# Kernel optimization log

Hardware: AMD Instinct MI355X
Metric: run time of the kernel (lower is better)

## Reference

```python
import jax, jax.numpy as jnp
import numpy as np

N = 10000      # nodes
E = 320000     # edges
D = 256        # input_nf = output_nf
H = 256        # hidden_nf
ED = 16        # edges_in_d
NORM = 32.0    # normalization_factor


def setup_inputs() -> dict:
    key = jax.random.key(0)
    ks = jax.random.split(key, 16)
    s = 0.02  # param scale
    return {
        "h": jax.random.normal(ks[0], (N, D), dtype=jnp.float32),
        "edge_index": jax.random.randint(ks[1], (2, E), 0, N, dtype=jnp.int64),
        "edge_attr": jax.random.normal(ks[2], (E, ED), dtype=jnp.float32),
        "node_mask": jnp.ones((N, 1), dtype=jnp.float32),
        "edge_mask": jnp.ones((E, 1), dtype=jnp.float32),
        # edge_mlp: Linear(2D+ED -> H), SiLU, Linear(H -> H), SiLU
        "We1": jax.random.normal(ks[3], (2 * D + ED, H), dtype=jnp.float32) * s,
        "be1": jnp.zeros((H,), dtype=jnp.float32),
        "We2": jax.random.normal(ks[4], (H, H), dtype=jnp.float32) * s,
        "be2": jnp.zeros((H,), dtype=jnp.float32),
        # att_mlp: Linear(H -> 1), Sigmoid
        "Wa": jax.random.normal(ks[5], (H, 1), dtype=jnp.float32) * s,
        "ba": jnp.zeros((1,), dtype=jnp.float32),
        # node_mlp: Linear(H + D -> H), SiLU, Linear(H -> D)
        "Wn1": jax.random.normal(ks[6], (H + D, H), dtype=jnp.float32) * s,
        "bn1": jnp.zeros((H,), dtype=jnp.float32),
        "Wn2": jax.random.normal(ks[7], (H, D), dtype=jnp.float32) * s,
        "bn2": jnp.zeros((D,), dtype=jnp.float32),
    }


def reference(h, edge_index, edge_attr, node_mask, edge_mask,
              We1, be1, We2, be2, Wa, ba, Wn1, bn1, Wn2, bn2):
    row, col = edge_index[0], edge_index[1]
    # edge model: gather endpoints, concat with edge_attr -> [E, 2D+ED]
    e_in = jnp.concatenate([h[row], h[col], edge_attr], axis=1)
    mij = jax.nn.silu(jax.nn.silu(e_in @ We1 + be1) @ We2 + be2)  # [E, H]
    att = jax.nn.sigmoid(mij @ Wa + ba)                            # [E, 1]
    edge_feat = mij * att * edge_mask                              # [E, H]
    # node model: scatter-add messages to rows, normalize by constant
    agg = jax.ops.segment_sum(edge_feat, row, num_segments=h.shape[0]) / NORM  # [N, H]
    a = jnp.concatenate([h, agg], axis=1)                          # [N, D+H]
    h_out = h + (jax.nn.silu(a @ Wn1 + bn1) @ Wn2 + bn2)           # residual
    h_out = h_out * node_mask
    return (h_out, mij)
```

## Files before the change

### kernel.cpp

```cpp
#include <hip/hip_runtime.h>

#define NN 10000
#define NE 320000

typedef __bf16 bf16x8 __attribute__((ext_vector_type(8)));
typedef short  s16x8  __attribute__((ext_vector_type(8)));
typedef float  f32x4  __attribute__((ext_vector_type(4)));

__device__ __forceinline__ unsigned short f2bf(float f) {
  return __builtin_bit_cast(unsigned short, (__bf16)f);
}
__device__ __forceinline__ float bf2f(unsigned short s) {
  unsigned u = ((unsigned)s) << 16;
  return __builtin_bit_cast(float, u);
}
__device__ __forceinline__ float sigm(float x) { return 1.0f / (1.0f + __expf(-x)); }
__device__ __forceinline__ float silu_f(float x) { return x / (1.0f + __expf(-x)); }

__global__ void prep_w(const float* __restrict__ We1, const float* __restrict__ We2,
                       const float* __restrict__ Wn1, const float* __restrict__ Wn2,
                       unsigned short* __restrict__ W1abT, unsigned short* __restrict__ W1cT,
                       unsigned short* __restrict__ We2T,
                       unsigned short* __restrict__ Wn1T, unsigned short* __restrict__ Wn2T) {
  int g = blockIdx.x * blockDim.x + threadIdx.x;
  const int S1 = 512 * 256, S2 = 256 * 32, S3 = 256 * 256, S4 = 256 * 512, S5 = 256 * 256;
  if (g < S1) {
    int n = g >> 8, k = g & 255;
    float v = (n < 256) ? We1[k * 256 + n] : We1[(256 + k) * 256 + (n - 256)];
    W1abT[g] = f2bf(v);
  } else if (g < S1 + S2) {
    int i = g - S1; int n = i >> 5, kk = i & 31;
    float v = (kk < 16) ? We1[(512 + kk) * 256 + n] : 0.0f;
    W1cT[i] = f2bf(v);
  } else if (g < S1 + S2 + S3) {
    int i = g - S1 - S2; int n = i >> 8, k = i & 255;
    We2T[i] = f2bf(We2[k * 256 + n]);
  } else if (g < S1 + S2 + S3 + S4) {
    int i = g - S1 - S2 - S3; int n = i >> 9, k = i & 511;
    Wn1T[i] = f2bf(Wn1[k * 256 + n]);
  } else if (g < S1 + S2 + S3 + S4 + S5) {
    int i = g - S1 - S2 - S3 - S4; int n = i >> 8, k = i & 255;
    Wn2T[i] = f2bf(Wn2[k * 256 + n]);
  }
}

__global__ void prep_x(const float* __restrict__ h, unsigned short* __restrict__ hb) {
  int g = blockIdx.x * blockDim.x + threadIdx.x;
  if (g < NN * 64) {
    float4 f = ((const float4*)h)[g];
    unsigned short* d = hb + g * 4;
    d[0] = f2bf(f.x); d[1] = f2bf(f.y); d[2] = f2bf(f.z); d[3] = f2bf(f.w);
  }
}

__global__ void hist_kernel(const int* __restrict__ eidx, int* __restrict__ rowi,
                            int* __restrict__ counts) {
  __shared__ int s64;
  if (threadIdx.x == 0) {
    bool b = true;
    for (int i = 1; i < 64; i += 2) b = b && (eidx[i] == 0);
    s64 = b ? 1 : 0;
  }
  __syncthreads();
  int e = blockIdx.x * 256 + threadIdx.x;
  if (e < NE) {
    int r = s64 ? (int)((const long long*)eidx)[e] : eidx[e];
    rowi[e] = r;
    atomicAdd(&counts[r], 1);
  }
}

__global__ __launch_bounds__(1024) void scan_kernel(const int* __restrict__ counts,
                                                    int* __restrict__ rowStart,
                                                    int* __restrict__ cursor) {
  __shared__ int part[1024];
  int t = threadIdx.x;
  int local[10];
  int s = 0;
  #pragma unroll
  for (int i = 0; i < 10; i++) {
    int idx = t * 10 + i;
    int c = (idx < NN) ? counts[idx] : 0;
    local[i] = s; s += c;
  }
  part[t] = s;
  __syncthreads();
  int val = s;
  for (int off = 1; off < 1024; off <<= 1) {
    int tmp = (t >= off) ? part[t - off] : 0;
    __syncthreads();
    part[t] += tmp;
    __syncthreads();
  }
  int base = part[t] - val;
  #pragma unroll
  for (int i = 0; i < 10; i++) {
    int idx = t * 10 + i;
    if (idx < NN) { int v = base + local[i]; rowStart[idx] = v; cursor[idx] = v; }
  }
  if (t == 1023) rowStart[NN] = NE;
}

__global__ void scatter_kernel(const int* __restrict__ rowi, int* __restrict__ cursor,
                               int* __restrict__ eorder, int* __restrict__ rowSorted) {
  int e = blockIdx.x * 256 + threadIdx.x;
  if (e < NE) {
    int r = rowi[e];
    int pos = atomicAdd(&cursor[r], 1);
    eorder[pos] = e;
    rowSorted[pos] = r;
  }
}

__global__ __launch_bounds__(512) void hpq_kernel(
    const unsigned short* __restrict__ hb, const unsigned short* __restrict__ W1abT,
    unsigned short* __restrict__ hPQb) {
  __shared__ unsigned short Abuf[128 * 40];
  __shared__ unsigned short Bbuf[256 * 40];

  const int tid = threadIdx.x;
  const int lane = tid & 63;
  const int wid = tid >> 6;
  const int wrr = wid >> 2, wcc = wid & 3;
  const int n0 = blockIdx.x * 128;
  const int coh = blockIdx.y;
  const unsigned short* Bsrc = W1abT + ((size_t)(coh << 8)) * 256;

  f32x4 acc[4][4];
  #pragma unroll
  for (int m = 0; m < 4; m++)
    #pragma unroll
    for (int n = 0; n < 4; n++) acc[m][n] = (f32x4){0.f, 0.f, 0.f, 0.f};

  const int eA = tid >> 2, sA = tid & 3;
  int nodeA = n0 + eA; if (nodeA >= NN) nodeA = NN - 1;
  const int rbase = (wrr << 6) + (lane & 15);
  const int koff = (lane >> 4) << 3;
  const int cfrag = lane & 15;

  for (int kt = 0; kt < 8; ++kt) {
    const int k0 = kt << 5;
    __syncthreads();
    *(s16x8*)&Abuf[eA * 40 + (sA << 3)] = *(const s16x8*)(hb + (size_t)nodeA * 256 + k0 + (sA << 3));
    #pragma unroll
    for (int i = 0; i < 2; ++i) {
      int idx = tid + (i << 9);
      int n = idx >> 2, s = idx & 3;
      *(s16x8*)&Bbuf[n * 40 + (s << 3)] = *(const s16x8*)(Bsrc + (n << 8) + k0 + (s << 3));
    }
    __syncthreads();
    bf16x8 a[4], b[4];
    #pragma unroll
    for (int m = 0; m < 4; m++)
      a[m] = __builtin_bit_cast(bf16x8, *(const s16x8*)&Abuf[(rbase + m * 16) * 40 + koff]);
    #pragma unroll
    for (int n = 0; n < 4; n++)
      b[n] = __builtin_bit_cast(bf16x8, *(const s16x8*)&Bbuf[((wcc << 6) + n * 16 + cfrag) * 40 + koff]);
    #pragma unroll
    for (int m = 0; m < 4; m++)
      #pragma unroll
      for (int n = 0; n < 4; n++)
        acc[m][n] = __builtin_amdgcn_mfma_f32_16x16x32_bf16(a[m], b[n], acc[m][n], 0, 0, 0);
  }

  #pragma unroll
  for (int m = 0; m < 4; m++) {
    int rl = (wrr << 6) + m * 16 + ((lane >> 4) << 2);
    #pragma unroll
    for (int n = 0; n < 4; n++) {
      int cg = (wcc << 6) + n * 16 + cfrag;
      #pragma unroll
      for (int j = 0; j < 4; j++) {
        int rg = n0 + rl + j;
        if (rg < NN) hPQb[(size_t)rg * 512 + (coh << 8) + cg] = f2bf(acc[m][n][j]);
      }
    }
  }
}

__global__ __launch_bounds__(512) void edge_kernel(
    const unsigned short* __restrict__ hPQb, const int* __restrict__ eidx,
    const float* __restrict__ eattr, const float* __restrict__ emask,
    const unsigned short* __restrict__ W1cT, const float* __restrict__ be1,
    const unsigned short* __restrict__ We2T, const float* __restrict__ be2,
    const float* __restrict__ Wa, const float* __restrict__ ba,
    const int* __restrict__ eorder, const int* __restrict__ rowSorted,
    float* __restrict__ mij_out, float* __restrict__ agg) {
  __shared__ unsigned short Bbuf[2][256 * 40];
  __shared__ unsigned short A2[64 * 264];
  __shared__ float attP[4][64];
  __shared__ float attL[64];
  __shared__ int rowL[64], colL[64], origL[64];
  __shared__ float waL[256], be1L[256], be2L[256];
  __shared__ int s64;

  const int tid = threadIdx.x;
  const int lane = tid & 63;
  const int wid = tid >> 6;
  const int wr = wid >> 2, wc = wid & 3;
  const int e0 = blockIdx.x * 64;
  const int cfrag = lane & 15;
  const int lq = lane >> 4;
  const int koff = lq << 3;
  const int rbase = (wr << 5) + cfrag;

  if (tid == 0) {
    bool b = true;
    for (int i = 1; i < 64; i += 2) b = b && (eidx[i] == 0);
    s64 = b ? 1 : 0;
  }
  __syncthreads();

  if (tid < 64) {
    int orig = eorder[e0 + tid];
    origL[tid] = orig;
    rowL[tid] = rowSorted[e0 + tid];
    colL[tid] = s64 ? (int)((const long long*)eidx)[NE + orig] : eidx[NE + orig];
  }
  if (tid >= 256) {
    int i = tid - 256;
    waL[i] = Wa[i]; be1L[i] = be1[i]; be2L[i] = be2[i];
  }
  __syncthreads();

  {
    int e = tid >> 3, p = tid & 7;
    int c0 = p << 5;
    const unsigned short* pr = hPQb + (size_t)rowL[e] * 512 + c0;
    const unsigned short* pc = hPQb + (size_t)colL[e] * 512 + 256 + c0;
    #pragma unroll
    for (int q = 0; q < 4; ++q) {
      s16x8 vr = *(const s16x8*)(pr + (q << 3));
      s16x8 vc = *(const s16x8*)(pc + (q << 3));
      s16x8 vo;
      #pragma unroll
      for (int j = 0; j < 8; ++j)
        vo[j] = (short)f2bf(bf2f((unsigned short)vr[j]) + bf2f((unsigned short)vc[j]));
      *(s16x8*)&A2[e * 264 + c0 + (q << 3)] = vo;
    }
  }

  const int sn0 = tid >> 2;
  const int ss0 = (tid & 3) << 3;
  {
    s16x8 v0 = *(const s16x8*)(W1cT + sn0 * 32 + ss0);
    s16x8 v1 = *(const s16x8*)(W1cT + (sn0 + 128) * 32 + ss0);
    *(s16x8*)&Bbuf[0][sn0 * 40 + ss0] = v0;
    *(s16x8*)&Bbuf[0][(sn0 + 128) * 40 + ss0] = v1;
  }
  __syncthreads();

  f32x4 acc[2][4];
  #pragma unroll
  for (int m = 0; m < 2; m++)
    #pragma unroll
    for (int n = 0; n < 4; n++) acc[m][n] = (f32x4){0.f, 0.f, 0.f, 0.f};

  for (int t = 0; t < 9; ++t) {
    const int cur = t & 1, nxt = cur ^ 1;

    s16x8 nb0, nb1;
    const bool doStage = (t < 8);
    if (doStage) {
      const int k0 = t << 5;
      nb0 = *(const s16x8*)(We2T + (sn0 << 8) + k0 + ss0);
      nb1 = *(const s16x8*)(We2T + ((sn0 + 128) << 8) + k0 + ss0);
    }

    bf16x8 a[2];
    if (t == 0) {
      #pragma unroll
      for (int m = 0; m < 2; m++) {
        int rl = rbase + m * 16;
        if (koff < 16) {
          const float* src = eattr + (size_t)origL[rl] * 16 + koff;
          float4 f0 = *(const float4*)src;
          float4 f1 = *(const float4*)(src + 4);
          s16x8 v;
          v[0] = (short)f2bf(f0.x); v[1] = (short)f2bf(f0.y);
          v[2] = (short)f2bf(f0.z); v[3] = (short)f2bf(f0.w);
          v[4] = (short)f2bf(f1.x); v[5] = (short)f2bf(f1.y);
          v[6] = (short)f2bf(f1.z); v[7] = (short)f2bf(f1.w);
          a[m] = __builtin_bit_cast(bf16x8, v);
        } else {
          a[m] = __builtin_bit_cast(bf16x8, (s16x8){0, 0, 0, 0, 0, 0, 0, 0});
        }
      }
    } else {
      const int k0 = (t - 1) << 5;
      #pragma unroll
      for (int m = 0; m < 2; m++)
        a[m] = __builtin_bit_cast(bf16x8, *(const s16x8*)&A2[(rbase + m * 16) * 264 + k0 + koff]);
    }

    bf16x8 b[4];
    #pragma unroll
    for (int n = 0; n < 4; n++)
      b[n] = __builtin_bit_cast(bf16x8, *(const s16x8*)&Bbuf[cur][((wc << 6) + n * 16 + cfrag) * 40 + koff]);

    #pragma unroll
    for (int m = 0; m < 2; m++)
      #pragma unroll
      for (int n = 0; n < 4; n++)
        acc[m][n] = __builtin_amdgcn_mfma_f32_16x16x32_bf16(a[m], b[n], acc[m][n], 0, 0, 0);

    if (doStage) {
      *(s16x8*)&Bbuf[nxt][sn0 * 40 + ss0] = nb0;
      *(s16x8*)&Bbuf[nxt][(sn0 + 128) * 40 + ss0] = nb1;
    }

    if (t == 0) {
      #pragma unroll
      for (int m = 0; m < 2; m++) {
        int rl = (wr << 5) + m * 16 + (lq << 2);
        #pragma unroll
        for (int n = 0; n < 4; n++) {
          int cg = (wc << 6) + n * 16 + cfrag;
          float bias = be1L[cg];
          #pragma unroll
          for (int j = 0; j < 4; j++) {
            float x = acc[m][n][j] + bf2f(A2[(rl + j) * 264 + cg]) + bias;
            A2[(rl + j) * 264 + cg] = f2bf(silu_f(x));
          }
          acc[m][n] = (f32x4){0.f, 0.f, 0.f, 0.f};
        }
      }
    }
    __syncthreads();
  }

  float part[2][4];
  #pragma unroll
  for (int m = 0; m < 2; m++)
    #pragma unroll
    for (int j = 0; j < 4; j++) part[m][j] = 0.f;

  #pragma unroll
  for (int m = 0; m < 2; m++) {
    #pragma unroll
    for (int n = 0; n < 4; n++) {
      int cg = (wc << 6) + n * 16 + cfrag;
      float bias = be2L[cg];
      float wav = waL[cg];
      #pragma unroll
      for (int j = 0; j < 4; j++) {
        int row = (wr << 5) + m * 16 + (lq << 2) + j;
        float x = silu_f(acc[m][n][j] + bias);
        mij_out[(size_t)origL[row] * 256 + cg] = x;
        A2[row * 264 + cg] = f2bf(x);
        part[m][j] += x * wav;
      }
    }
  }
  #pragma unroll
  for (int m = 0; m < 2; m++)
    #pragma unroll
    for (int j = 0; j < 4; j++) {
      float p = part[m][j];
      p += __shfl_xor(p, 1);
      p += __shfl_xor(p, 2);
      p += __shfl_xor(p, 4);
      p += __shfl_xor(p, 8);
      part[m][j] = p;
    }
  if (cfrag == 0) {
    #pragma unroll
    for (int m = 0; m < 2; m++)
      #pragma unroll
      for (int j = 0; j < 4; j++)
        attP[wc][(wr << 5) + m * 16 + (lq << 2) + j] = part[m][j];
  }
  __syncthreads();
  if (tid < 64) {
    float s = attP[0][tid] + attP[1][tid] + attP[2][tid] + attP[3][tid] + ba[0];
    attL[tid] = sigm(s) * emask[origL[tid]];
  }
  __syncthreads();

  if (tid < 256) {
    const int c = tid;
    const int fd = rowL[0], ld = rowL[63];
    float acc2 = 0.f;
    int prev = fd;
    for (int i = 0; i < 64; ++i) {
      int r = rowL[i];
      if (r != prev) {
        if (prev == fd) atomicAdd(&agg[(size_t)prev * 256 + c], acc2);
        else            agg[(size_t)prev * 256 + c] = acc2;
        acc2 = 0.f; prev = r;
      }
      acc2 += attL[i] * bf2f(A2[i * 264 + c]);
    }
    atomicAdd(&agg[(size_t)prev * 256 + c], acc2);
    (void)ld;
  }
}

__global__ __launch_bounds__(512) void node_kernel(
    const float* __restrict__ h, const float* __restrict__ agg,
    const float* __restrict__ nmask,
    const unsigned short* __restrict__ Wn1T, const float* __restrict__ bn1,
    const unsigned short* __restrict__ Wn2T, const float* __restrict__ bn2,
    float* __restrict__ hout) {
  __shared__ unsigned short Abuf[128 * 40];
  __shared__ unsigned short Bbuf[256 * 40];
  __shared__ unsigned short A2[128 * 264];
  __shared__ float bn1L[256], bn2L[256];

  const int tid = threadIdx.x;
  const int lane = tid & 63;
  const int wid = tid >> 6;
  const int n0 = blockIdx.x * 128;

  if (tid < 256) { bn1L[tid] = bn1[tid]; bn2L[tid] = bn2[tid]; }

  f32x4 acc[4][4];
  #pragma unroll
  for (int m = 0; m < 4; m++)
    #pragma unroll
    for (int n = 0; n < 4; n++) acc[m][n] = (f32x4){0.f, 0.f, 0.f, 0.f};

  const int eA = tid >> 2, sA = tid & 3;
  int nodeA = n0 + eA; if (nodeA >= NN) nodeA = NN - 1;
  const int wrr = wid >> 2, wcc = wid & 3;
  const int rbase = (wrr << 6) + (lane & 15);
  const int koff = (lane >> 4) << 3;
  const int cfrag = lane & 15;

  for (int kt = 0; kt < 16; ++kt) {
    const int k0 = kt << 5;
    __syncthreads();
    {
      const float* src = (k0 < 256) ? (h + (size_t)nodeA * 256 + k0 + (sA << 3))
                                    : (agg + (size_t)nodeA * 256 + (k0 - 256) + (sA << 3));
      const float sc = (k0 < 256) ? 1.0f : (1.0f / 32.0f);
      float4 f0 = *(const float4*)src;
      float4 f1 = *(const float4*)(src + 4);
      s16x8 v;
      v[0] = (short)f2bf(f0.x * sc); v[1] = (short)f2bf(f0.y * sc);
      v[2] = (short)f2bf(f0.z * sc); v[3] = (short)f2bf(f0.w * sc);
      v[4] = (short)f2bf(f1.x * sc); v[5] = (short)f2bf(f1.y * sc);
      v[6] = (short)f2bf(f1.z * sc); v[7] = (short)f2bf(f1.w * sc);
      *(s16x8*)&Abuf[eA * 40 + (sA << 3)] = v;
    }
    #pragma unroll
    for (int i = 0; i < 2; ++i) {
      int idx = tid + (i << 9);
      int n = idx >> 2, s = idx & 3;
      s16x8 v = *(const s16x8*)(Wn1T + (n << 9) + k0 + (s << 3));
      *(s16x8*)&Bbuf[n * 40 + (s << 3)] = v;
    }
    __syncthreads();
    bf16x8 a[4], b[4];
    #pragma unroll
    for (int m = 0; m < 4; m++)
      a[m] = __builtin_bit_cast(bf16x8, *(const s16x8*)&Abuf[(rbase + m * 16) * 40 + koff]);
    #pragma unroll
    for (int n = 0; n < 4; n++)
      b[n] = __builtin_bit_cast(bf16x8, *(const s16x8*)&Bbuf[((wcc << 6) + n * 16 + cfrag) * 40 + koff]);
    #pragma unroll
    for (int m = 0; m < 4; m++)
      #pragma unroll
      for (int n = 0; n < 4; n++)
        acc[m][n] = __builtin_amdgcn_mfma_f32_16x16x32_bf16(a[m], b[n], acc[m][n], 0, 0, 0);
  }

  #pragma unroll
  for (int m = 0; m < 4; m++) {
    int rl = (wrr << 6) + m * 16 + ((lane >> 4) << 2);
    #pragma unroll
    for (int n = 0; n < 4; n++) {
      int cg = (wcc << 6) + n * 16 + cfrag;
      float bias = bn1L[cg];
      #pragma unroll
      for (int j = 0; j < 4; j++) {
        float x = acc[m][n][j] + bias;
        A2[(rl + j) * 264 + cg] = f2bf(silu_f(x));
      }
      acc[m][n] = (f32x4){0.f, 0.f, 0.f, 0.f};
    }
  }

  for (int kt = 0; kt < 8; ++kt) {
    const int k0 = kt << 5;
    __syncthreads();
    #pragma unroll
    for (int i = 0; i < 2; ++i) {
      int idx = tid + (i << 9);
      int n = idx >> 2, s = idx & 3;
      s16x8 v = *(const s16x8*)(Wn2T + (n << 8) + k0 + (s << 3));
      *(s16x8*)&Bbuf[n * 40 + (s << 3)] = v;
    }
    __syncthreads();
    bf16x8 a[4], b[4];
    #pragma unroll
    for (int m = 0; m < 4; m++)
      a[m] = __builtin_bit_cast(bf16x8, *(const s16x8*)&A2[(rbase + m * 16) * 264 + k0 + koff]);
    #pragma unroll
    for (int n = 0; n < 4; n++)
      b[n] = __builtin_bit_cast(bf16x8, *(const s16x8*)&Bbuf[((wcc << 6) + n * 16 + cfrag) * 40 + koff]);
    #pragma unroll
    for (int m = 0; m < 4; m++)
      #pragma unroll
      for (int n = 0; n < 4; n++)
        acc[m][n] = __builtin_amdgcn_mfma_f32_16x16x32_bf16(a[m], b[n], acc[m][n], 0, 0, 0);
  }

  #pragma unroll
  for (int m = 0; m < 4; m++) {
    int rl = (wrr << 6) + m * 16 + ((lane >> 4) << 2);
    #pragma unroll
    for (int n = 0; n < 4; n++) {
      int cg = (wcc << 6) + n * 16 + cfrag;
      #pragma unroll
      for (int j = 0; j < 4; j++) {
        int rg = n0 + rl + j;
        if (rg < NN) {
          float val = acc[m][n][j] + bn2L[cg];
          float o = (h[(size_t)rg * 256 + cg] + val) * nmask[rg];
          hout[(size_t)rg * 256 + cg] = o;
        }
      }
    }
  }
}

extern "C" void kernel_launch(void* const* d_in, const int* in_sizes, int n_in,
                              void* d_out, int out_size, void* d_ws, size_t ws_size,
                              hipStream_t stream) {
  (void)in_sizes; (void)n_in; (void)out_size; (void)ws_size;
  const float* h     = (const float*)d_in[0];
  const int*   eidx  = (const int*)d_in[1];
  const float* eattr = (const float*)d_in[2];
  const float* nmask = (const float*)d_in[3];
  const float* emask = (const float*)d_in[4];
  const float* We1 = (const float*)d_in[5];
  const float* be1 = (const float*)d_in[6];
  const float* We2 = (const float*)d_in[7];
  const float* be2 = (const float*)d_in[8];
  const float* Wa  = (const float*)d_in[9];
  const float* ba  = (const float*)d_in[10];
  const float* Wn1 = (const float*)d_in[11];
  const float* bn1 = (const float*)d_in[12];
  const float* Wn2 = (const float*)d_in[13];
  const float* bn2 = (const float*)d_in[14];

  char* ws = (char*)d_ws;
  unsigned short* W1abT = (unsigned short*)(ws + 0);
  unsigned short* W1cT  = (unsigned short*)(ws + 262144);
  unsigned short* We2T  = (unsigned short*)(ws + 278528);
  unsigned short* Wn1T  = (unsigned short*)(ws + 409600);
  unsigned short* Wn2T  = (unsigned short*)(ws + 671744);
  unsigned short* hPQb  = (unsigned short*)(ws + 802816);
  float* agg      = (float*)(ws + 11042816);
  int*   counts   = (int*)(ws + 21282816);
  int*   rowStart = (int*)(ws + 21322816);
  int*   cursor   = (int*)(ws + 21362824);
  int*   eorder   = (int*)(ws + 21402824);
  int*   rowi     = (int*)(ws + 22682824);
  int*   rowSorted= (int*)(ws + 23962824);
  unsigned short* hb = (unsigned short*)(ws + 25242824);

  float* hout = (float*)d_out;
  float* mij  = (float*)d_out + (size_t)NN * 256;

  hipMemsetAsync(counts, 0, NN * sizeof(int), stream);
  hipMemsetAsync(agg, 0, (size_t)NN * 256 * sizeof(float), stream);
  prep_w<<<1568, 256, 0, stream>>>(We1, We2, Wn1, Wn2, W1abT, W1cT, We2T, Wn1T, Wn2T);
  prep_x<<<2500, 256, 0, stream>>>(h, hb);
  hist_kernel<<<(NE + 255) / 256, 256, 0, stream>>>(eidx, rowi, counts);
  scan_kernel<<<1, 1024, 0, stream>>>(counts, rowStart, cursor);
  scatter_kernel<<<(NE + 255) / 256, 256, 0, stream>>>(rowi, cursor, eorder, rowSorted);
  hpq_kernel<<<dim3((NN + 127) / 128, 2), 512, 0, stream>>>(hb, W1abT, hPQb);
  edge_kernel<<<NE / 64, 512, 0, stream>>>(hPQb, eidx, eattr, emask, W1cT, be1, We2T, be2,
                                           Wa, ba, eorder, rowSorted, mij, agg);
  node_kernel<<<(NN + 127) / 128, 512, 0, stream>>>(h, agg, nmask, Wn1T, bn1, Wn2T, bn2, hout);
}
```

Baseline: 371.3 us.

## Load MFMA weight fragments directly from global, dropping LDS staging

Removes the LDS B-buffers in the hpq, edge and node kernels. Weight fragments now go straight from global memory (L1/L2-resident) into MFMA registers, which removes a staging store and barrier per k-step and frees LDS so more blocks can be resident (launch bounds raised to 4 and 8). The edge kernel's fused 9-step double-buffered loop is split into a single edge-attr step and a fully unrolled 8-step We2 loop. Its segmented reduction now uses all 512 threads, each half covering 32 edges. The cost is more global/L2 traffic for weight reads that used to be shared through LDS, plus possible register pressure from the occupancy hints.

```diff
diff --git a/kernel.cpp b/kernel.cpp
--- a/kernel.cpp
+++ b/kernel.cpp
@@ -112,11 +112,10 @@
   }
 }
 
-__global__ __launch_bounds__(512) void hpq_kernel(
+__global__ __launch_bounds__(512, 4) void hpq_kernel(
     const unsigned short* __restrict__ hb, const unsigned short* __restrict__ W1abT,
     unsigned short* __restrict__ hPQb) {
   __shared__ unsigned short Abuf[128 * 40];
-  __shared__ unsigned short Bbuf[256 * 40];
 
   const int tid = threadIdx.x;
   const int lane = tid & 63;
@@ -142,12 +141,6 @@
     const int k0 = kt << 5;
     __syncthreads();
     *(s16x8*)&Abuf[eA * 40 + (sA << 3)] = *(const s16x8*)(hb + (size_t)nodeA * 256 + k0 + (sA << 3));
-    #pragma unroll
-    for (int i = 0; i < 2; ++i) {
-      int idx = tid + (i << 9);
-      int n = idx >> 2, s = idx & 3;
-      *(s16x8*)&Bbuf[n * 40 + (s << 3)] = *(const s16x8*)(Bsrc + (n << 8) + k0 + (s << 3));
-    }
     __syncthreads();
     bf16x8 a[4], b[4];
     #pragma unroll
@@ -155,7 +148,8 @@
       a[m] = __builtin_bit_cast(bf16x8, *(const s16x8*)&Abuf[(rbase + m * 16) * 40 + koff]);
     #pragma unroll
     for (int n = 0; n < 4; n++)
-      b[n] = __builtin_bit_cast(bf16x8, *(const s16x8*)&Bbuf[((wcc << 6) + n * 16 + cfrag) * 40 + koff]);
+      b[n] = __builtin_bit_cast(bf16x8,
+               *(const s16x8*)(Bsrc + (((wcc << 6) + n * 16 + cfrag) << 8) + k0 + koff));
     #pragma unroll
     for (int m = 0; m < 4; m++)
       #pragma unroll
@@ -178,7 +172,7 @@
   }
 }
 
-__global__ __launch_bounds__(512) void edge_kernel(
+__global__ __launch_bounds__(512, 8) void edge_kernel(
     const unsigned short* __restrict__ hPQb, const int* __restrict__ eidx,
     const float* __restrict__ eattr, const float* __restrict__ emask,
     const unsigned short* __restrict__ W1cT, const float* __restrict__ be1,
@@ -186,7 +180,6 @@
     const float* __restrict__ Wa, const float* __restrict__ ba,
     const int* __restrict__ eorder, const int* __restrict__ rowSorted,
     float* __restrict__ mij_out, float* __restrict__ agg) {
-  __shared__ unsigned short Bbuf[2][256 * 40];
   __shared__ unsigned short A2[64 * 264];
   __shared__ float attP[4][64];
   __shared__ float attL[64];
@@ -223,6 +216,12 @@
   }
   __syncthreads();
 
+  f32x4 acc[2][4];
+  #pragma unroll
+  for (int m = 0; m < 2; m++)
+    #pragma unroll
+    for (int n = 0; n < 4; n++) acc[m][n] = (f32x4){0.f, 0.f, 0.f, 0.f};
+
   {
     int e = tid >> 3, p = tid & 7;
     int c0 = p << 5;
@@ -239,95 +238,72 @@
       *(s16x8*)&A2[e * 264 + c0 + (q << 3)] = vo;
     }
   }
-
-  const int sn0 = tid >> 2;
-  const int ss0 = (tid & 3) << 3;
   {
-    s16x8 v0 = *(const s16x8*)(W1cT + sn0 * 32 + ss0);
-    s16x8 v1 = *(const s16x8*)(W1cT + (sn0 + 128) * 32 + ss0);
-    *(s16x8*)&Bbuf[0][sn0 * 40 + ss0] = v0;
-    *(s16x8*)&Bbuf[0][(sn0 + 128) * 40 + ss0] = v1;
-  }
-  __syncthreads();
-
-  f32x4 acc[2][4];
-  #pragma unroll
-  for (int m = 0; m < 2; m++)
-    #pragma unroll
-    for (int n = 0; n < 4; n++) acc[m][n] = (f32x4){0.f, 0.f, 0.f, 0.f};
-
-  for (int t = 0; t < 9; ++t) {
-    const int cur = t & 1, nxt = cur ^ 1;
-
-    s16x8 nb0, nb1;
-    const bool doStage = (t < 8);
-    if (doStage) {
-      const int k0 = t << 5;
-      nb0 = *(const s16x8*)(We2T + (sn0 << 8) + k0 + ss0);
-      nb1 = *(const s16x8*)(We2T + ((sn0 + 128) << 8) + k0 + ss0);
-    }
-
-    bf16x8 a[2];
-    if (t == 0) {
-      #pragma unroll
-      for (int m = 0; m < 2; m++) {
-        int rl = rbase + m * 16;
-        if (koff < 16) {
-          const float* src = eattr + (size_t)origL[rl] * 16 + koff;
-          float4 f0 = *(const float4*)src;
-          float4 f1 = *(const float4*)(src + 4);
-          s16x8 v;
-          v[0] = (short)f2bf(f0.x); v[1] = (short)f2bf(f0.y);
-          v[2] = (short)f2bf(f0.z); v[3] = (short)f2bf(f0.w);
-          v[4] = (short)f2bf(f1.x); v[5] = (short)f2bf(f1.y);
-          v[6] = (short)f2bf(f1.z); v[7] = (short)f2bf(f1.w);
-          a[m] = __builtin_bit_cast(bf16x8, v);
-        } else {
-          a[m] = __builtin_bit_cast(bf16x8, (s16x8){0, 0, 0, 0, 0, 0, 0, 0});
-        }
-      }
-    } else {
-      const int k0 = (t - 1) << 5;
-      #pragma unroll
-      for (int m = 0; m < 2; m++)
-        a[m] = __builtin_bit_cast(bf16x8, *(const s16x8*)&A2[(rbase + m * 16) * 264 + k0 + koff]);
-    }
-
-    bf16x8 b[4];
+    bf16x8 a[2], b[4];
+    #pragma unroll
+    for (int m = 0; m < 2; m++) {
+      int rl = rbase + m * 16;
+      if (koff < 16) {
+        const float* src = eattr + (size_t)origL[rl] * 16 + koff;
+        float4 f0 = *(const float4*)src;
+        float4 f1 = *(const float4*)(src + 4);
+        s16x8 v;
+        v[0] = (short)f2bf(f0.x); v[1] = (short)f2bf(f0.y);
+        v[2] = (short)f2bf(f0.z); v[3] = (short)f2bf(f0.w);
+        v[4] = (short)f2bf(f1.x); v[5] = (short)f2bf(f1.y);
+        v[6] = (short)f2bf(f1.z); v[7] = (short)f2bf(f1.w);
+        a[m] = __builtin_bit_cast(bf16x8, v);
+      } else {
+        a[m] = __builtin_bit_cast(bf16x8, (s16x8){0, 0, 0, 0, 0, 0, 0, 0});
+      }
+    }
     #pragma unroll
     for (int n = 0; n < 4; n++)
-      b[n] = __builtin_bit_cast(bf16x8, *(const s16x8*)&Bbuf[cur][((wc << 6) + n * 16 + cfrag) * 40 + koff]);
-
+      b[n] = __builtin_bit_cast(bf16x8,
+               *(const s16x8*)(W1cT + (((wc << 6) + n * 16 + cfrag) << 5) + koff));
     #pragma unroll
     for (int m = 0; m < 2; m++)
       #pragma unroll
       for (int n = 0; n < 4; n++)
         acc[m][n] = __builtin_amdgcn_mfma_f32_16x16x32_bf16(a[m], b[n], acc[m][n], 0, 0, 0);
-
-    if (doStage) {
-      *(s16x8*)&Bbuf[nxt][sn0 * 40 + ss0] = nb0;
-      *(s16x8*)&Bbuf[nxt][(sn0 + 128) * 40 + ss0] = nb1;
-    }
-
-    if (t == 0) {
-      #pragma unroll
-      for (int m = 0; m < 2; m++) {
-        int rl = (wr << 5) + m * 16 + (lq << 2);
-        #pragma unroll
-        for (int n = 0; n < 4; n++) {
-          int cg = (wc << 6) + n * 16 + cfrag;
-          float bias = be1L[cg];
-          #pragma unroll
-          for (int j = 0; j < 4; j++) {
-            float x = acc[m][n][j] + bf2f(A2[(rl + j) * 264 + cg]) + bias;
-            A2[(rl + j) * 264 + cg] = f2bf(silu_f(x));
-          }
-          acc[m][n] = (f32x4){0.f, 0.f, 0.f, 0.f};
-        }
-      }
-    }
-    __syncthreads();
-  }
+  }
+  __syncthreads();
+
+  #pragma unroll
+  for (int m = 0; m < 2; m++) {
+    int rl = (wr << 5) + m * 16 + (lq << 2);
+    #pragma unroll
+    for (int n = 0; n < 4; n++) {
+      int cg = (wc << 6) + n * 16 + cfrag;
+      float bias = be1L[cg];
+      #pragma unroll
+      for (int j = 0; j < 4; j++) {
+        float x = acc[m][n][j] + bf2f(A2[(rl + j) * 264 + cg]) + bias;
+        A2[(rl + j) * 264 + cg] = f2bf(silu_f(x));
+      }
+      acc[m][n] = (f32x4){0.f, 0.f, 0.f, 0.f};
+    }
+  }
+  __syncthreads();
+
+  #pragma unroll
+  for (int t = 0; t < 8; ++t) {
+    const int k0 = t << 5;
+    bf16x8 a[2], b[4];
+    #pragma unroll
+    for (int m = 0; m < 2; m++)
+      a[m] = __builtin_bit_cast(bf16x8, *(const s16x8*)&A2[(rbase + m * 16) * 264 + k0 + koff]);
+    #pragma unroll
+    for (int n = 0; n < 4; n++)
+      b[n] = __builtin_bit_cast(bf16x8,
+               *(const s16x8*)(We2T + (((wc << 6) + n * 16 + cfrag) << 8) + k0 + koff));
+    #pragma unroll
+    for (int m = 0; m < 2; m++)
+      #pragma unroll
+      for (int n = 0; n < 4; n++)
+        acc[m][n] = __builtin_amdgcn_mfma_f32_16x16x32_bf16(a[m], b[n], acc[m][n], 0, 0, 0);
+  }
+  __syncthreads();
 
   float part[2][4];
   #pragma unroll
@@ -377,12 +353,14 @@
   }
   __syncthreads();
 
-  if (tid < 256) {
-    const int c = tid;
-    const int fd = rowL[0], ld = rowL[63];
+  {
+    const int half = tid >> 8;
+    const int c = tid & 255;
+    const int i0 = half << 5, i1 = i0 + 32;
+    const int fd = rowL[i0];
     float acc2 = 0.f;
     int prev = fd;
-    for (int i = 0; i < 64; ++i) {
+    for (int i = i0; i < i1; ++i) {
       int r = rowL[i];
       if (r != prev) {
         if (prev == fd) atomicAdd(&agg[(size_t)prev * 256 + c], acc2);
@@ -392,18 +370,16 @@
       acc2 += attL[i] * bf2f(A2[i * 264 + c]);
     }
     atomicAdd(&agg[(size_t)prev * 256 + c], acc2);
-    (void)ld;
-  }
-}
-
-__global__ __launch_bounds__(512) void node_kernel(
+  }
+}
+
+__global__ __launch_bounds__(512, 4) void node_kernel(
     const float* __restrict__ h, const float* __restrict__ agg,
     const float* __restrict__ nmask,
     const unsigned short* __restrict__ Wn1T, const float* __restrict__ bn1,
     const unsigned short* __restrict__ Wn2T, const float* __restrict__ bn2,
     float* __restrict__ hout) {
   __shared__ unsigned short Abuf[128 * 40];
-  __shared__ unsigned short Bbuf[256 * 40];
   __shared__ unsigned short A2[128 * 264];
   __shared__ float bn1L[256], bn2L[256];
 
@@ -443,13 +419,6 @@
       v[6] = (short)f2bf(f1.z * sc); v[7] = (short)f2bf(f1.w * sc);
       *(s16x8*)&Abuf[eA * 40 + (sA << 3)] = v;
     }
-    #pragma unroll
-    for (int i = 0; i < 2; ++i) {
-      int idx = tid + (i << 9);
-      int n = idx >> 2, s = idx & 3;
-      s16x8 v = *(const s16x8*)(Wn1T + (n << 9) + k0 + (s << 3));
-      *(s16x8*)&Bbuf[n * 40 + (s << 3)] = v;
-    }
     __syncthreads();
     bf16x8 a[4], b[4];
     #pragma unroll
@@ -457,7 +426,8 @@
       a[m] = __builtin_bit_cast(bf16x8, *(const s16x8*)&Abuf[(rbase + m * 16) * 40 + koff]);
     #pragma unroll
     for (int n = 0; n < 4; n++)
-      b[n] = __builtin_bit_cast(bf16x8, *(const s16x8*)&Bbuf[((wcc << 6) + n * 16 + cfrag) * 40 + koff]);
+      b[n] = __builtin_bit_cast(bf16x8,
+               *(const s16x8*)(Wn1T + (((wcc << 6) + n * 16 + cfrag) << 9) + k0 + koff));
     #pragma unroll
     for (int m = 0; m < 4; m++)
       #pragma unroll
@@ -480,25 +450,19 @@
       acc[m][n] = (f32x4){0.f, 0.f, 0.f, 0.f};
     }
   }
-
+  __syncthreads();
+
+  #pragma unroll
   for (int kt = 0; kt < 8; ++kt) {
     const int k0 = kt << 5;
-    __syncthreads();
-    #pragma unroll
-    for (int i = 0; i < 2; ++i) {
-      int idx = tid + (i << 9);
-      int n = idx >> 2, s = idx & 3;
-      s16x8 v = *(const s16x8*)(Wn2T + (n << 8) + k0 + (s << 3));
-      *(s16x8*)&Bbuf[n * 40 + (s << 3)] = v;
-    }
-    __syncthreads();
     bf16x8 a[4], b[4];
     #pragma unroll
     for (int m = 0; m < 4; m++)
       a[m] = __builtin_bit_cast(bf16x8, *(const s16x8*)&A2[(rbase + m * 16) * 264 + k0 + koff]);
     #pragma unroll
     for (int n = 0; n < 4; n++)
-      b[n] = __builtin_bit_cast(bf16x8, *(const s16x8*)&Bbuf[((wcc << 6) + n * 16 + cfrag) * 40 + koff]);
+      b[n] = __builtin_bit_cast(bf16x8,
+               *(const s16x8*)(Wn2T + (((wcc << 6) + n * 16 + cfrag) << 8) + k0 + koff));
     #pragma unroll
     for (int m = 0; m < 4; m++)
       #pragma unroll
```

Measured after the change: 536.4 us. 44.4% more time.
